# Optimization experiments

Hardware: AMD Instinct MI355X
Metric: run time of the kernel (lower is better)

The kernel has to match this reference:

```python
import jax, jax.numpy as jnp
import numpy as np
import math

B, TT, TS, C, H, L = 8, 256, 512, 512, 8, 10
HD = C // H
TOPK_FRAME = 64
# layer schedule mirrors MultimodalTransformer.forward tower order:
# 4 stimulus cross-attn (kv=frames, topk), 2 causal self-attn, 2 history cross-attn, 2 causal self-attn
# kv_source: 0=frames, 1=self, 2=id_prev
SCHED = [(0, False, TOPK_FRAME)] * 4 + [(1, True, None)] * 2 + [(2, False, None)] * 2 + [(1, True, None)] * 2


def setup_inputs() -> dict:
    key = jax.random.key(0)
    ks = jax.random.split(key, 4)
    kws = jax.random.split(ks[3], 6)
    w = lambda k, s: jax.random.normal(k, s, jnp.float32) * 0.02
    return {
        "id_x": jax.random.normal(ks[0], (B, TT, C), jnp.float32),
        "id_prev": jax.random.normal(ks[1], (B, TT, C), jnp.float32),
        "frames": jax.random.normal(ks[2], (B, TS, C), jnp.float32),
        "Wq": w(kws[0], (L, C, C)), "bq": jnp.zeros((L, C), jnp.float32),
        "Wk": w(kws[1], (L, C, C)), "bk": jnp.zeros((L, C), jnp.float32),
        "Wv": w(kws[2], (L, C, C)), "bv": jnp.zeros((L, C), jnp.float32),
        "Wo": w(kws[3], (L, C, C)), "bo": jnp.zeros((L, C), jnp.float32),
        "W1": w(kws[4], (L, C, 4 * C)), "b1": jnp.zeros((L, 4 * C), jnp.float32),
        "W2": w(kws[5], (L, 4 * C, C)), "b2": jnp.zeros((L, C), jnp.float32),
        "ln1_g": jnp.ones((L, C), jnp.float32), "ln1_b": jnp.zeros((L, C), jnp.float32),
        "ln2_g": jnp.ones((L, C), jnp.float32), "ln2_b": jnp.zeros((L, C), jnp.float32),
        "lnf_g": jnp.ones((L, C), jnp.float32), "lnf_b": jnp.zeros((L, C), jnp.float32),
    }


def _ln(x, g, b):
    mu = x.mean(-1, keepdims=True)
    var = ((x - mu) ** 2).mean(-1, keepdims=True)
    return (x - mu) * jax.lax.rsqrt(var + 1e-5) * g + b


def _block(x, kv, causal, topk, p):
    # Block.forward: x = x + attn(ln1(x), kv, kv, mask); x = x + mlp(ln2(x)); return ln_f(x)
    Wq, bq, Wk, bk, Wv, bv, Wo, bo, W1, b1, W2, b2, l1g, l1b, l2g, l2b, lfg, lfb = p
    Bx, Tt, Cx = x.shape
    Ts = kv.shape[1]
    h = _ln(x, l1g, l1b)
    q = (h @ Wq + bq).reshape(Bx, Tt, H, HD).transpose(0, 2, 1, 3)   # [B,H,Tt,HD]
    k = (kv @ Wk + bk).reshape(Bx, Ts, H, HD).transpose(0, 2, 1, 3)  # [B,H,Ts,HD]
    v = (kv @ Wv + bv).reshape(Bx, Ts, H, HD).transpose(0, 2, 1, 3)
    att = jnp.einsum('bhqd,bhkd->bhqk', q, k) * (1.0 / math.sqrt(HD))
    if causal:
        m = jnp.tril(jnp.ones((Tt, Ts), dtype=bool))
        att = jnp.where(m, att, -jnp.inf)
    if topk is not None and topk < Ts:
        top = jax.lax.top_k(att, topk)[0]           # [B,H,Tt,topk]
        att = jnp.where(att < top[..., -1:], -jnp.inf, att)
    w_att = jax.nn.softmax(att, axis=-1)
    y = jnp.einsum('bhqk,bhkd->bhqd', w_att, v).transpose(0, 2, 1, 3).reshape(Bx, Tt, Cx)
    x = x + y @ Wo + bo
    h2 = _ln(x, l2g, l2b)
    x = x + jax.nn.gelu(h2 @ W1 + b1, approximate=False) @ W2 + b2
    return _ln(x, lfg, lfb)


def _forward(id_x, id_prev, frames, Wq, bq, Wk, bk, Wv, bv, Wo, bo, W1, b1, W2, b2,
             ln1_g, ln1_b, ln2_g, ln2_b, lnf_g, lnf_b):
    x = id_x
    for i, (src, causal, topk) in enumerate(SCHED):
        kv = (frames, x, id_prev)[src]
        p = (Wq[i], bq[i], Wk[i], bk[i], Wv[i], bv[i], Wo[i], bo[i],
             W1[i], b1[i], W2[i], b2[i],
             ln1_g[i], ln1_b[i], ln2_g[i], ln2_b[i], lnf_g[i], lnf_b[i])
        x = _block(x, kv, causal, topk, p)
    return x


def reference(id_x, id_prev, frames, Wq, bq, Wk, bk, Wv, bv, Wo, bo, W1, b1, W2, b2,
              ln1_g, ln1_b, ln2_g, ln2_b, lnf_g, lnf_b):
    return _forward(id_x, id_prev, frames, Wq, bq, Wk, bk, Wv, bv, Wo, bo, W1, b1, W2, b2,
                    ln1_g, ln1_b, ln2_g, ln2_b, lnf_g, lnf_b)
```

## Files before the change

### kernel.cpp

```cpp
#include <hip/hip_runtime.h>
#include <math.h>

#define CC 512
#define NH 8
#define HD 64
#define TT 256

typedef __attribute__((ext_vector_type(8))) short short8v;
typedef __attribute__((ext_vector_type(4))) float f32x4;

__device__ inline unsigned short bfc(float f) {
  unsigned u = __float_as_uint(f);
  return (unsigned short)((u + 0x7fffu + ((u >> 16) & 1u)) >> 16);
}
__device__ inline float b2f(unsigned short s) {
  return __uint_as_float((unsigned)s << 16);
}
__device__ inline void gld16(const void* g, void* l) {
  __builtin_amdgcn_global_load_lds(
      (const __attribute__((address_space(1))) unsigned int*)g,
      (__attribute__((address_space(3))) unsigned int*)l, 16, 0, 0);
}

__global__ __launch_bounds__(256) void prep_k(const float* __restrict__ id_x,
    const float* __restrict__ frames, const float* __restrict__ id_prev,
    float* __restrict__ x, unsigned short* __restrict__ fb,
    unsigned short* __restrict__ pb) {
  int i = blockIdx.x * 256 + threadIdx.x;
  if (i < 262144) {
    ((float4*)x)[i] = ((const float4*)id_x)[i];
  } else if (i < 786432) {
    int j = i - 262144;
    float4 f = ((const float4*)frames)[j];
    ushort4 o; o.x = bfc(f.x); o.y = bfc(f.y); o.z = bfc(f.z); o.w = bfc(f.w);
    ((ushort4*)fb)[j] = o;
  } else {
    int j = i - 786432;
    float4 f = ((const float4*)id_prev)[j];
    ushort4 o; o.x = bfc(f.x); o.y = bfc(f.y); o.z = bfc(f.z); o.w = bfc(f.w);
    ((ushort4*)pb)[j] = o;
  }
}

__global__ __launch_bounds__(256) void ln_bf(const float* __restrict__ in,
    unsigned short* __restrict__ out, const float* __restrict__ g, const float* __restrict__ b) {
  int row = (blockIdx.x << 2) + (threadIdx.x >> 6), lane = threadIdx.x & 63;
  const float* r = in + (size_t)row * CC;
  float4 v0 = *(const float4*)(r + (lane << 2));
  float4 v1 = *(const float4*)(r + 256 + (lane << 2));
  float s = v0.x + v0.y + v0.z + v0.w + v1.x + v1.y + v1.z + v1.w;
  #pragma unroll
  for (int o = 32; o; o >>= 1) s += __shfl_xor(s, o);
  float mu = s * (1.0f / CC);
  float d0x = v0.x - mu, d0y = v0.y - mu, d0z = v0.z - mu, d0w = v0.w - mu;
  float d1x = v1.x - mu, d1y = v1.y - mu, d1z = v1.z - mu, d1w = v1.w - mu;
  float sq = d0x*d0x + d0y*d0y + d0z*d0z + d0w*d0w + d1x*d1x + d1y*d1y + d1z*d1z + d1w*d1w;
  #pragma unroll
  for (int o = 32; o; o >>= 1) sq += __shfl_xor(sq, o);
  float inv = rsqrtf(sq * (1.0f / CC) + 1e-5f);
  float4 g0 = *(const float4*)(g + (lane << 2)), g1 = *(const float4*)(g + 256 + (lane << 2));
  float4 b0 = *(const float4*)(b + (lane << 2)), b1 = *(const float4*)(b + 256 + (lane << 2));
  ushort4 o0, o1;
  o0.x = bfc(d0x*inv*g0.x + b0.x); o0.y = bfc(d0y*inv*g0.y + b0.y);
  o0.z = bfc(d0z*inv*g0.z + b0.z); o0.w = bfc(d0w*inv*g0.w + b0.w);
  o1.x = bfc(d1x*inv*g1.x + b1.x); o1.y = bfc(d1y*inv*g1.y + b1.y);
  o1.z = bfc(d1z*inv*g1.z + b1.z); o1.w = bfc(d1w*inv*g1.w + b1.w);
  *(ushort4*)(out + (size_t)row * CC + (lane << 2)) = o0;
  *(ushort4*)(out + (size_t)row * CC + 256 + (lane << 2)) = o1;
}

__global__ __launch_bounds__(256) void ln_final(const float* __restrict__ in,
    float* __restrict__ out, const float* __restrict__ g, const float* __restrict__ b) {
  int row = (blockIdx.x << 2) + (threadIdx.x >> 6), lane = threadIdx.x & 63;
  const float* r = in + (size_t)row * CC;
  float4 v0 = *(const float4*)(r + (lane << 2));
  float4 v1 = *(const float4*)(r + 256 + (lane << 2));
  float s = v0.x + v0.y + v0.z + v0.w + v1.x + v1.y + v1.z + v1.w;
  #pragma unroll
  for (int o = 32; o; o >>= 1) s += __shfl_xor(s, o);
  float mu = s * (1.0f / CC);
  float d0x = v0.x - mu, d0y = v0.y - mu, d0z = v0.z - mu, d0w = v0.w - mu;
  float d1x = v1.x - mu, d1y = v1.y - mu, d1z = v1.z - mu, d1w = v1.w - mu;
  float sq = d0x*d0x + d0y*d0y + d0z*d0z + d0w*d0w + d1x*d1x + d1y*d1y + d1z*d1z + d1w*d1w;
  #pragma unroll
  for (int o = 32; o; o >>= 1) sq += __shfl_xor(sq, o);
  float inv = rsqrtf(sq * (1.0f / CC) + 1e-5f);
  float4 g0 = *(const float4*)(g + (lane << 2)), g1 = *(const float4*)(g + 256 + (lane << 2));
  float4 b0 = *(const float4*)(b + (lane << 2)), b1 = *(const float4*)(b + 256 + (lane << 2));
  float4 o0, o1;
  o0.x = d0x*inv*g0.x + b0.x; o0.y = d0y*inv*g0.y + b0.y;
  o0.z = d0z*inv*g0.z + b0.z; o0.w = d0w*inv*g0.w + b0.w;
  o1.x = d1x*inv*g1.x + b1.x; o1.y = d1y*inv*g1.y + b1.y;
  o1.z = d1z*inv*g1.z + b1.z; o1.w = d1w*inv*g1.w + b1.w;
  *(float4*)(out + (size_t)row * CC + (lane << 2)) = o0;
  *(float4*)(out + (size_t)row * CC + 256 + (lane << 2)) = o1;
}

__global__ __launch_bounds__(256) void ln_chain(const float* __restrict__ in,
    float* __restrict__ xout, unsigned short* __restrict__ xb,
    const float* __restrict__ gf, const float* __restrict__ bf,
    const float* __restrict__ g1, const float* __restrict__ b1,
    unsigned short* __restrict__ hout) {
  int row = (blockIdx.x << 2) + (threadIdx.x >> 6), lane = threadIdx.x & 63;
  const float* r = in + (size_t)row * CC;
  float4 v0 = *(const float4*)(r + (lane << 2));
  float4 v1 = *(const float4*)(r + 256 + (lane << 2));
  float s = v0.x + v0.y + v0.z + v0.w + v1.x + v1.y + v1.z + v1.w;
  #pragma unroll
  for (int o = 32; o; o >>= 1) s += __shfl_xor(s, o);
  float mu = s * (1.0f / CC);
  float d0x = v0.x - mu, d0y = v0.y - mu, d0z = v0.z - mu, d0w = v0.w - mu;
  float d1x = v1.x - mu, d1y = v1.y - mu, d1z = v1.z - mu, d1w = v1.w - mu;
  float sq = d0x*d0x + d0y*d0y + d0z*d0z + d0w*d0w + d1x*d1x + d1y*d1y + d1z*d1z + d1w*d1w;
  #pragma unroll
  for (int o = 32; o; o >>= 1) sq += __shfl_xor(sq, o);
  float inv = rsqrtf(sq * (1.0f / CC) + 1e-5f);
  float4 g0 = *(const float4*)(gf + (lane << 2)), g1v = *(const float4*)(gf + 256 + (lane << 2));
  float4 b0 = *(const float4*)(bf + (lane << 2)), b1v = *(const float4*)(bf + 256 + (lane << 2));
  float4 x0, x1;
  x0.x = d0x*inv*g0.x + b0.x; x0.y = d0y*inv*g0.y + b0.y;
  x0.z = d0z*inv*g0.z + b0.z; x0.w = d0w*inv*g0.w + b0.w;
  x1.x = d1x*inv*g1v.x + b1v.x; x1.y = d1y*inv*g1v.y + b1v.y;
  x1.z = d1z*inv*g1v.z + b1v.z; x1.w = d1w*inv*g1v.w + b1v.w;
  *(float4*)(xout + (size_t)row * CC + (lane << 2)) = x0;
  *(float4*)(xout + (size_t)row * CC + 256 + (lane << 2)) = x1;
  ushort4 xb0, xb1;
  xb0.x = bfc(x0.x); xb0.y = bfc(x0.y); xb0.z = bfc(x0.z); xb0.w = bfc(x0.w);
  xb1.x = bfc(x1.x); xb1.y = bfc(x1.y); xb1.z = bfc(x1.z); xb1.w = bfc(x1.w);
  *(ushort4*)(xb + (size_t)row * CC + (lane << 2)) = xb0;
  *(ushort4*)(xb + (size_t)row * CC + 256 + (lane << 2)) = xb1;
  float s2 = x0.x + x0.y + x0.z + x0.w + x1.x + x1.y + x1.z + x1.w;
  #pragma unroll
  for (int o = 32; o; o >>= 1) s2 += __shfl_xor(s2, o);
  float mu2 = s2 * (1.0f / CC);
  float e0x = x0.x - mu2, e0y = x0.y - mu2, e0z = x0.z - mu2, e0w = x0.w - mu2;
  float e1x = x1.x - mu2, e1y = x1.y - mu2, e1z = x1.z - mu2, e1w = x1.w - mu2;
  float sq2 = e0x*e0x + e0y*e0y + e0z*e0z + e0w*e0w + e1x*e1x + e1y*e1y + e1z*e1z + e1w*e1w;
  #pragma unroll
  for (int o = 32; o; o >>= 1) sq2 += __shfl_xor(sq2, o);
  float inv2 = rsqrtf(sq2 * (1.0f / CC) + 1e-5f);
  float4 h0 = *(const float4*)(g1 + (lane << 2)), h1 = *(const float4*)(g1 + 256 + (lane << 2));
  float4 c0 = *(const float4*)(b1 + (lane << 2)), c1 = *(const float4*)(b1 + 256 + (lane << 2));
  ushort4 ho0, ho1;
  ho0.x = bfc(e0x*inv2*h0.x + c0.x); ho0.y = bfc(e0y*inv2*h0.y + c0.y);
  ho0.z = bfc(e0z*inv2*h0.z + c0.z); ho0.w = bfc(e0w*inv2*h0.w + c0.w);
  ho1.x = bfc(e1x*inv2*h1.x + c1.x); ho1.y = bfc(e1y*inv2*h1.y + c1.y);
  ho1.z = bfc(e1z*inv2*h1.z + c1.z); ho1.w = bfc(e1w*inv2*h1.w + c1.w);
  *(ushort4*)(hout + (size_t)row * CC + (lane << 2)) = ho0;
  *(ushort4*)(hout + (size_t)row * CC + 256 + (lane << 2)) = ho1;
}

__global__ __launch_bounds__(256) void transpose_w(
    const float* __restrict__ Wq, const float* __restrict__ Wk,
    const float* __restrict__ Wv, const float* __restrict__ Wo,
    const float* __restrict__ W1, const float* __restrict__ W2,
    int layer_base, unsigned short* __restrict__ wT) {
  int lz = blockIdx.x / 3072;
  int layer = layer_base + lz;
  int bid = blockIdx.x - lz * 3072;
  unsigned short* wTl = wT + (size_t)lz * 3145728;
  const float* src; unsigned short* dst; int R, Cn, tile, lg;
  if (bid < 1024) {
    int seg = bid >> 8; tile = bid & 255; R = 512; Cn = 512; lg = 4;
    const float* s4[4] = {Wq, Wk, Wv, Wo};
    src = s4[seg] + (size_t)layer * 262144;
    dst = wTl + (size_t)seg * 262144;
  } else if (bid < 2048) {
    tile = bid - 1024; R = 512; Cn = 2048; lg = 6;
    src = W1 + (size_t)layer * 1048576; dst = wTl + 1048576;
  } else {
    tile = bid - 2048; R = 2048; Cn = 512; lg = 4;
    src = W2 + (size_t)layer * 1048576; dst = wTl + 2097152;
  }
  int trb = tile >> lg, tcb = tile & ((1 << lg) - 1);
  __shared__ float tl[32][33];
  int t = threadIdx.x;
  int r = t >> 3, c4 = (t & 7) << 2;
  const float* sp = src + (size_t)(trb * 32 + r) * Cn + tcb * 32 + c4;
  float4 fv = *(const float4*)sp;
  tl[r][c4] = fv.x; tl[r][c4 + 1] = fv.y; tl[r][c4 + 2] = fv.z; tl[r][c4 + 3] = fv.w;
  __syncthreads();
  unsigned short* dp = dst + (size_t)(tcb * 32 + r) * R + trb * 32 + c4;
  ushort4 ov;
  ov.x = bfc(tl[c4][r]); ov.y = bfc(tl[c4 + 1][r]);
  ov.z = bfc(tl[c4 + 2][r]); ov.w = bfc(tl[c4 + 3][r]);
  *(ushort4*)dp = ov;
}

template<int BM, int GELU, int RES, int OUTBF, int BIAS2>
__global__ __launch_bounds__(256) void gemm_bf(
    const unsigned short* __restrict__ A, const unsigned short* __restrict__ WT,
    const float* __restrict__ bias, const float* __restrict__ bias2,
    void* __restrict__ outp, const float* __restrict__ res, int M, int N, int K) {
  __shared__ __align__(16) unsigned short As[BM * 64];
  __shared__ __align__(16) unsigned short Bs[64 * 64];
  const int tid = threadIdx.x, lane = tid & 63, wid = tid >> 6;
  const int bm = blockIdx.y * BM, bn = blockIdx.x << 6;
  const int wm = (wid >> 1) * (BM / 2), wn = (wid & 1) << 5;
  constexpr int MF = BM / 32;
  f32x4 acc[MF][2] = {};
  const int fr = lane & 15, fq = lane >> 4;
  for (int k0 = 0; k0 < K; k0 += 64) {
    if (k0) __syncthreads();
    #pragma unroll
    for (int i = 0; i < BM / 32; i++) {
      int gl = tid + (i << 8);
      int row = gl >> 3, gc = gl & 7;
      int gcs = gc ^ (row & 7);
      gld16(A + (size_t)(bm + row) * K + k0 + (gcs << 3),
            (char*)As + (i << 12) + (wid << 10));
    }
    #pragma unroll
    for (int i = 0; i < 2; i++) {
      int gl = tid + (i << 8);
      int row = gl >> 3, gc = gl & 7;
      int gcs = gc ^ (row & 7);
      gld16(WT + (size_t)(bn + row) * K + k0 + (gcs << 3),
            (char*)Bs + (i << 12) + (wid << 10));
    }
    __syncthreads();
    short8v af[MF][2], bf2[2][2];
    #pragma unroll
    for (int mf = 0; mf < MF; mf++)
      #pragma unroll
      for (int ks = 0; ks < 2; ks++) {
        int r = wm + mf * 16 + fr;
        int c = (ks << 2) + fq;
        af[mf][ks] = *(const short8v*)((const char*)As + ((((r << 7) + (c << 4))) ^ ((r & 7) << 4)));
      }
    #pragma unroll
    for (int nf = 0; nf < 2; nf++)
      #pragma unroll
      for (int ks = 0; ks < 2; ks++) {
        int r = wn + nf * 16 + fr;
        int c = (ks << 2) + fq;
        bf2[nf][ks] = *(const short8v*)((const char*)Bs + ((((r << 7) + (c << 4))) ^ ((r & 7) << 4)));
      }
    #pragma unroll
    for (int mf = 0; mf < MF; mf++)
      #pragma unroll
      for (int nf = 0; nf < 2; nf++) {
        acc[mf][nf] = __builtin_amdgcn_mfma_f32_16x16x32_bf16(af[mf][0], bf2[nf][0], acc[mf][nf], 0, 0, 0);
        acc[mf][nf] = __builtin_amdgcn_mfma_f32_16x16x32_bf16(af[mf][1], bf2[nf][1], acc[mf][nf], 0, 0, 0);
      }
  }
  #pragma unroll
  for (int mf = 0; mf < MF; mf++)
    #pragma unroll
    for (int nf = 0; nf < 2; nf++) {
      int col = bn + wn + nf * 16 + fr;
      float bia = (BIAS2 && col >= 512) ? bias2[col - 512] : bias[col];
      #pragma unroll
      for (int rr = 0; rr < 4; rr++) {
        int row = bm + wm + mf * 16 + fq * 4 + rr;
        float vv = acc[mf][nf][rr] + bia;
        if (GELU) vv = 0.5f * vv * (1.0f + erff(vv * 0.70710678118654752f));
        if (RES)  vv += res[(size_t)row * N + col];
        if (OUTBF) ((unsigned short*)outp)[(size_t)row * N + col] = bfc(vv);
        else       ((float*)outp)[(size_t)row * N + col] = vv;
      }
    }
}

template<int CAUSAL, int TOPK, int TSK>
__global__ __launch_bounds__(512, 4) void attn_m(
    const unsigned short* __restrict__ qb, const unsigned short* __restrict__ kv,
    unsigned short* __restrict__ yb) {
  constexpr int NT = TSK / 64;
  constexpr int NKC = TSK / 128;
  constexpr int SST = TSK + 8;
  __shared__ float S[8 * SST];
  __shared__ __align__(16) unsigned short Ks[128 * 64];
  __shared__ __align__(16) unsigned short Qs[16 * 64];
  __shared__ float swt[TOPK ? 8 : 1][TOPK ? 128 : 1];
  __shared__ unsigned short kidx[TOPK ? 8 : 1][TOPK ? 128 : 1];
  int tid = threadIdx.x, lane = tid & 63, wid = tid >> 6;
  int bid = blockIdx.x;
  int swz = ((bid & 7) << 8) | (bid >> 3);
  int b = swz >> 8, h = (swz >> 5) & 7, q0 = (swz & 31) << 3;
  if (tid < 128) {
    int row = tid >> 3, gc = tid & 7;
    short8v o8 = {0, 0, 0, 0, 0, 0, 0, 0};
    if (row < 8) {
      const unsigned short* qsrc = qb + (size_t)((b << 8) + q0 + row) * CC + (h << 6) + (gc << 3);
      short8v raw = *(const short8v*)qsrc;
      #pragma unroll
      for (int e = 0; e < 8; e++)
        o8[e] = (short)bfc(b2f((unsigned short)raw[e]) * 0.125f);
    }
    *(short8v*)((char*)Qs + ((tid << 4) ^ ((row & 7) << 4))) = o8;
  }
  __syncthreads();
  short8v aF[2];
  {
    int r = lane & 15, kq2 = lane >> 4;
    #pragma unroll
    for (int kc2 = 0; kc2 < 2; kc2++)
      aF[kc2] = *(const short8v*)((const char*)Qs +
                 (((r << 7) + (kc2 << 6) + (kq2 << 4)) ^ ((r & 7) << 4)));
  }
  int nte = NKC;
  if (CAUSAL) { int ub = (q0 + 8 + 127) >> 7; nte = ub < NKC ? ub : NKC; }
  const unsigned short* kgb = kv + (size_t)b * TSK * 1024 + (h << 6);
  for (int t = 0; t < nte; t++) {
    __syncthreads();
    #pragma unroll
    for (int j = 0; j < 2; j++) {
      int s = (wid << 7) + (j << 6) + lane;
      int row = s >> 3, sp = s & 7;
      gld16(kgb + (size_t)((t << 7) + row) * 1024 + ((sp ^ (row & 7)) << 3),
            (char*)Ks + (wid << 11) + (j << 10));
    }
    __syncthreads();
    int kq2 = lane >> 4;
    f32x4 acc = {};
    int key16 = (wid << 4) + (lane & 15);
    #pragma unroll
    for (int kc2 = 0; kc2 < 2; kc2++) {
      short8v bF = *(const short8v*)((const char*)Ks +
                    (((key16 << 7) + (kc2 << 6) + (kq2 << 4)) ^ ((key16 & 7) << 4)));
      acc = __builtin_amdgcn_mfma_f32_16x16x32_bf16(aF[kc2], bF, acc, 0, 0, 0);
    }
    if (kq2 < 2) {
      int col = (t << 7) + key16;
      #pragma unroll
      for (int r = 0; r < 4; r++)
        S[(kq2 * 4 + r) * SST + col] = acc[r];
    }
  }
  __syncthreads();
  int row = wid;
  int qi = q0 + row;
  int jmax = CAUSAL ? (qi + 1) : TSK;
  const unsigned short* vgb = kv + (size_t)b * TSK * 1024 + 512 + (h << 6) + lane;
  float sc[NT];
  float lmax = -3.0e38f;
  #pragma unroll
  for (int tt = 0; tt < NT; tt++) {
    int key = lane + (tt << 6);
    float v = (!CAUSAL || key < jmax) ? S[row * SST + key] : -3.0e38f;
    sc[tt] = v;
    lmax = fmaxf(lmax, v);
  }
  float mx = lmax;
  #pragma unroll
  for (int o = 32; o; o >>= 1) mx = fmaxf(mx, __shfl_xor(mx, o));
  float oacc = 0.f;
  if (TOPK) {
    unsigned key[NT];
    #pragma unroll
    for (int tt = 0; tt < NT; tt++) {
      unsigned u = __float_as_uint(sc[tt]);
      key[tt] = (u & 0x80000000u) ? ~u : (u | 0x80000000u);
    }
    unsigned prefix = 0u;
    for (int bit = 31; bit >= 0; bit--) {
      unsigned cand = prefix | (1u << bit);
      int cnt = 0;
      #pragma unroll
      for (int tt = 0; tt < NT; tt++)
        cnt += __popcll(__ballot(key[tt] >= cand));
      if (cnt >= 64) {
        prefix = cand;
        if (cnt == 64) break;
      }
    }
    float wvv[NT];
    float psum = 0.f;
    int basec = 0;
    #pragma unroll
    for (int tt = 0; tt < NT; tt++) {
      bool keep = key[tt] >= prefix;
      float wv = keep ? exp2f((sc[tt] - mx) * 1.4426950408889634f) : 0.f;
      wvv[tt] = wv;
      psum += wv;
      unsigned long long mask = __ballot(keep);
      if (keep) {
        int pos = basec + (int)__popcll(mask & ((1ull << lane) - 1ull));
        if (pos < 128) {
          kidx[row][pos] = (unsigned short)(lane + (tt << 6));
          swt[row][pos] = wv;
        }
      }
      basec += (int)__popcll(mask);
    }
    #pragma unroll
    for (int o = 32; o; o >>= 1) psum += __shfl_xor(psum, o);
    float inv = 1.0f / psum;
    int nk = basec;
    if (nk <= 128) {
      float a0 = 0.f, a1 = 0.f, a2 = 0.f, a3 = 0.f;
      int i = 0;
      for (; i + 3 < nk; i += 4) {
        a0 += swt[row][i]     * b2f(vgb[(size_t)kidx[row][i] * 1024]);
        a1 += swt[row][i + 1] * b2f(vgb[(size_t)kidx[row][i + 1] * 1024]);
        a2 += swt[row][i + 2] * b2f(vgb[(size_t)kidx[row][i + 2] * 1024]);
        a3 += swt[row][i + 3] * b2f(vgb[(size_t)kidx[row][i + 3] * 1024]);
      }
      for (; i < nk; i++) a0 += swt[row][i] * b2f(vgb[(size_t)kidx[row][i] * 1024]);
      oacc = (a0 + a1 + a2 + a3) * inv;
    } else {
      #pragma unroll
      for (int tt = 0; tt < NT; tt++)
        S[row * SST + lane + (tt << 6)] = wvv[tt];
      float a0 = 0.f, a1 = 0.f;
      for (int j = 0; j + 1 < TSK; j += 2) {
        a0 += S[row * SST + j]     * b2f(vgb[(size_t)j * 1024]);
        a1 += S[row * SST + j + 1] * b2f(vgb[(size_t)(j + 1) * 1024]);
      }
      oacc = (a0 + a1) * inv;
    }
  } else {
    float psum = 0.f;
    #pragma unroll
    for (int tt = 0; tt < NT; tt++) {
      int keyj = lane + (tt << 6);
      float wv = (keyj < jmax) ? exp2f((sc[tt] - mx) * 1.4426950408889634f) : 0.f;
      S[row * SST + keyj] = wv;
      psum += wv;
    }
    #pragma unroll
    for (int o = 32; o; o >>= 1) psum += __shfl_xor(psum, o);
    float inv = 1.0f / psum;
    float a0 = 0.f, a1 = 0.f, a2 = 0.f, a3 = 0.f;
    int j = 0;
    for (; j + 3 < jmax; j += 4) {
      a0 += S[row * SST + j]     * b2f(vgb[(size_t)j * 1024]);
      a1 += S[row * SST + j + 1] * b2f(vgb[(size_t)(j + 1) * 1024]);
      a2 += S[row * SST + j + 2] * b2f(vgb[(size_t)(j + 2) * 1024]);
      a3 += S[row * SST + j + 3] * b2f(vgb[(size_t)(j + 3) * 1024]);
    }
    for (; j < jmax; j++) a0 += S[row * SST + j] * b2f(vgb[(size_t)j * 1024]);
    oacc = (a0 + a1 + a2 + a3) * inv;
  }
  yb[(size_t)((b << 8) + qi) * CC + (h << 6) + lane] = bfc(oacc);
}

extern "C" void kernel_launch(void* const* d_in, const int* in_sizes, int n_in,
                              void* d_out, int out_size, void* d_ws, size_t ws_size,
                              hipStream_t stream) {
  const float* id_x    = (const float*)d_in[0];
  const float* id_prev = (const float*)d_in[1];
  const float* frames  = (const float*)d_in[2];
  const float* Wq = (const float*)d_in[3];  const float* bq = (const float*)d_in[4];
  const float* Wk = (const float*)d_in[5];  const float* bk = (const float*)d_in[6];
  const float* Wv = (const float*)d_in[7];  const float* bv = (const float*)d_in[8];
  const float* Wo = (const float*)d_in[9];  const float* bo = (const float*)d_in[10];
  const float* W1 = (const float*)d_in[11]; const float* b1 = (const float*)d_in[12];
  const float* W2 = (const float*)d_in[13]; const float* b2 = (const float*)d_in[14];
  const float* l1g = (const float*)d_in[15]; const float* l1b = (const float*)d_in[16];
  const float* l2g = (const float*)d_in[17]; const float* l2b = (const float*)d_in[18];
  const float* lfg = (const float*)d_in[19]; const float* lfb = (const float*)d_in[20];

  float* x = (float*)d_out;
  char* W  = (char*)d_ws;
  unsigned short* qbuf = (unsigned short*)W;
  unsigned short* kvb  = (unsigned short*)(W + ((size_t)4  << 20));
  unsigned short* m1b  = (unsigned short*)(W + ((size_t)4  << 20));
  unsigned short* hb   = (unsigned short*)(W + ((size_t)12 << 20));
  unsigned short* ybf  = (unsigned short*)(W + ((size_t)14 << 20));
  unsigned short* xb   = (unsigned short*)(W + ((size_t)16 << 20));
  unsigned short* fb   = (unsigned short*)(W + ((size_t)18 << 20));
  unsigned short* pb   = (unsigned short*)(W + ((size_t)22 << 20));
  unsigned short* wT   = (unsigned short*)(W + ((size_t)24 << 20));

  const bool allw = ws_size >= (((size_t)24 << 20) + (size_t)10 * 3145728 * 2);

  prep_k<<<4096, 256, 0, stream>>>(id_x, frames, id_prev, x, fb, pb);
  if (allw)
    transpose_w<<<30720, 256, 0, stream>>>(Wq, Wk, Wv, Wo, W1, W2, 0, wT);

  static const int ssrc[10] = {0, 0, 0, 0, 1, 1, 2, 2, 1, 1};

  for (int i = 0; i < 10; i++) {
    if (!allw)
      transpose_w<<<3072, 256, 0, stream>>>(Wq, Wk, Wv, Wo, W1, W2, i, wT);
    unsigned short* wTl = wT + (allw ? (size_t)i * 3145728 : 0);
    unsigned short* wqT = wTl;
    unsigned short* wkvT = wTl + 262144;
    unsigned short* woT = wTl + 786432;
    unsigned short* w1T = wTl + 1048576;
    unsigned short* w2T = wTl + 2097152;

    if (i == 0)
      ln_bf<<<512, 256, 0, stream>>>(x, hb, l1g, l1b);

    gemm_bf<32, 0, 0, 1, 0><<<dim3(8, 64), 256, 0, stream>>>(hb, wqT, bq + i * 512, nullptr, qbuf, nullptr, 2048, 512, 512);

    const unsigned short* kvsrc; int Mkv;
    if (ssrc[i] == 0)      { kvsrc = fb; Mkv = 4096; }
    else if (ssrc[i] == 1) { kvsrc = xb; Mkv = 2048; }
    else                   { kvsrc = pb; Mkv = 2048; }
    if (Mkv == 4096)
      gemm_bf<64, 0, 0, 1, 1><<<dim3(16, 64), 256, 0, stream>>>(kvsrc, wkvT, bk + i * 512, bv + i * 512, kvb, nullptr, 4096, 1024, 512);
    else
      gemm_bf<32, 0, 0, 1, 1><<<dim3(16, 64), 256, 0, stream>>>(kvsrc, wkvT, bk + i * 512, bv + i * 512, kvb, nullptr, 2048, 1024, 512);

    if (ssrc[i] == 0)      attn_m<0, 1, 512><<<2048, 512, 0, stream>>>(qbuf, kvb, ybf);
    else if (ssrc[i] == 1) attn_m<1, 0, 256><<<2048, 512, 0, stream>>>(qbuf, kvb, ybf);
    else                   attn_m<0, 0, 256><<<2048, 512, 0, stream>>>(qbuf, kvb, ybf);

    gemm_bf<32, 0, 1, 0, 0><<<dim3(8, 64), 256, 0, stream>>>(ybf, woT, bo + i * 512, nullptr, x, x, 2048, 512, 512);
    ln_bf<<<512, 256, 0, stream>>>(x, hb, l2g + i * 512, l2b + i * 512);
    gemm_bf<64, 1, 0, 1, 0><<<dim3(32, 32), 256, 0, stream>>>(hb, w1T, b1 + i * 2048, nullptr, m1b, nullptr, 2048, 2048, 512);
    gemm_bf<32, 0, 1, 0, 0><<<dim3(8, 64), 256, 0, stream>>>(m1b, w2T, b2 + i * 512, nullptr, x, x, 2048, 512, 2048);

    if (i < 9)
      ln_chain<<<512, 256, 0, stream>>>(x, x, xb, lfg + i * 512, lfb + i * 512,
                                        l1g + (i + 1) * 512, l1b + (i + 1) * 512, hb);
    else
      ln_final<<<512, 256, 0, stream>>>(x, x, lfg + i * 512, lfb + i * 512);
  }
}
```

Baseline: 1.006 ms.

## Double-buffer GEMM LDS staging, fold Q scaling into GEMM, enlarge transpose tiles

The GEMM kernel now uses two LDS buffers and issues the async global-to-LDS loads for the next K tile before computing the current one. This overlaps memory traffic with MFMA work and removes one barrier per iteration, at the cost of doubled shared memory, which may reduce occupancy. The 1/sqrt(HD) query scaling moves into the Q-projection GEMM epilogue, so the attention kernel loads Q straight to LDS with global_load_lds instead of converting in registers. The weight-transpose kernel switches from 32x32 to 64x64 tiles, cutting the block count fourfold.

```diff
diff --git a/kernel.cpp b/kernel.cpp
--- a/kernel.cpp
+++ b/kernel.cpp
@@ -155,70 +155,83 @@
     const float* __restrict__ Wv, const float* __restrict__ Wo,
     const float* __restrict__ W1, const float* __restrict__ W2,
     int layer_base, unsigned short* __restrict__ wT) {
-  int lz = blockIdx.x / 3072;
+  int lz = blockIdx.x / 768;
   int layer = layer_base + lz;
-  int bid = blockIdx.x - lz * 3072;
+  int bid = blockIdx.x - lz * 768;
   unsigned short* wTl = wT + (size_t)lz * 3145728;
-  const float* src; unsigned short* dst; int R, Cn, tile, lg;
-  if (bid < 1024) {
-    int seg = bid >> 8; tile = bid & 255; R = 512; Cn = 512; lg = 4;
+  const float* src; unsigned short* dst; int R, Cn, tile, lgc;
+  if (bid < 256) {
+    int seg = bid >> 6; tile = bid & 63; R = 512; Cn = 512; lgc = 3;
     const float* s4[4] = {Wq, Wk, Wv, Wo};
     src = s4[seg] + (size_t)layer * 262144;
     dst = wTl + (size_t)seg * 262144;
-  } else if (bid < 2048) {
-    tile = bid - 1024; R = 512; Cn = 2048; lg = 6;
+  } else if (bid < 512) {
+    tile = bid - 256; R = 512; Cn = 2048; lgc = 5;
     src = W1 + (size_t)layer * 1048576; dst = wTl + 1048576;
   } else {
-    tile = bid - 2048; R = 2048; Cn = 512; lg = 4;
+    tile = bid - 512; R = 2048; Cn = 512; lgc = 3;
     src = W2 + (size_t)layer * 1048576; dst = wTl + 2097152;
   }
-  int trb = tile >> lg, tcb = tile & ((1 << lg) - 1);
-  __shared__ float tl[32][33];
+  int trb = tile >> lgc, tcb = tile & ((1 << lgc) - 1);
+  __shared__ float tl[64][65];
   int t = threadIdx.x;
-  int r = t >> 3, c4 = (t & 7) << 2;
-  const float* sp = src + (size_t)(trb * 32 + r) * Cn + tcb * 32 + c4;
-  float4 fv = *(const float4*)sp;
-  tl[r][c4] = fv.x; tl[r][c4 + 1] = fv.y; tl[r][c4 + 2] = fv.z; tl[r][c4 + 3] = fv.w;
+  int r = t >> 2, c0 = (t & 3) << 4;
+  const float* sp = src + (size_t)(trb * 64 + r) * Cn + tcb * 64 + c0;
+  #pragma unroll
+  for (int j = 0; j < 4; j++) {
+    float4 fv = *(const float4*)(sp + (j << 2));
+    tl[r][c0 + (j << 2)]     = fv.x; tl[r][c0 + (j << 2) + 1] = fv.y;
+    tl[r][c0 + (j << 2) + 2] = fv.z; tl[r][c0 + (j << 2) + 3] = fv.w;
+  }
   __syncthreads();
-  unsigned short* dp = dst + (size_t)(tcb * 32 + r) * R + trb * 32 + c4;
-  ushort4 ov;
-  ov.x = bfc(tl[c4][r]); ov.y = bfc(tl[c4 + 1][r]);
-  ov.z = bfc(tl[c4 + 2][r]); ov.w = bfc(tl[c4 + 3][r]);
-  *(ushort4*)dp = ov;
-}
-
-template<int BM, int GELU, int RES, int OUTBF, int BIAS2>
+  unsigned short* dp = dst + (size_t)(tcb * 64 + r) * R + trb * 64 + c0;
+  #pragma unroll
+  for (int j = 0; j < 4; j++) {
+    ushort4 ov;
+    ov.x = bfc(tl[c0 + (j << 2)][r]);     ov.y = bfc(tl[c0 + (j << 2) + 1][r]);
+    ov.z = bfc(tl[c0 + (j << 2) + 2][r]); ov.w = bfc(tl[c0 + (j << 2) + 3][r]);
+    *(ushort4*)(dp + (j << 2)) = ov;
+  }
+}
+
+template<int BM, int GELU, int RES, int OUTBF, int BIAS2, int QSC>
 __global__ __launch_bounds__(256) void gemm_bf(
     const unsigned short* __restrict__ A, const unsigned short* __restrict__ WT,
     const float* __restrict__ bias, const float* __restrict__ bias2,
     void* __restrict__ outp, const float* __restrict__ res, int M, int N, int K) {
-  __shared__ __align__(16) unsigned short As[BM * 64];
-  __shared__ __align__(16) unsigned short Bs[64 * 64];
+  __shared__ __align__(16) unsigned short As[2][BM * 64];
+  __shared__ __align__(16) unsigned short Bs[2][64 * 64];
   const int tid = threadIdx.x, lane = tid & 63, wid = tid >> 6;
   const int bm = blockIdx.y * BM, bn = blockIdx.x << 6;
   const int wm = (wid >> 1) * (BM / 2), wn = (wid & 1) << 5;
   constexpr int MF = BM / 32;
   f32x4 acc[MF][2] = {};
   const int fr = lane & 15, fq = lane >> 4;
+  const int srow_a = tid >> 3, sgc = tid & 7;
+  const int sgcs = sgc ^ (srow_a & 7);
+
+  auto stage = [&](int buf, int k0) {
+    #pragma unroll
+    for (int i = 0; i < BM / 32; i++) {
+      int row = srow_a + (i << 5);
+      int gcs = sgc ^ (row & 7);
+      gld16(A + (size_t)(bm + row) * K + k0 + (gcs << 3),
+            (char*)As[buf] + (i << 12) + (wid << 10));
+    }
+    #pragma unroll
+    for (int i = 0; i < 2; i++) {
+      int row = srow_a + (i << 5);
+      int gcs = sgc ^ (row & 7);
+      gld16(WT + (size_t)(bn + row) * K + k0 + (gcs << 3),
+            (char*)Bs[buf] + (i << 12) + (wid << 10));
+    }
+  };
+
+  stage(0, 0);
+  __syncthreads();
+  int cur = 0;
   for (int k0 = 0; k0 < K; k0 += 64) {
-    if (k0) __syncthreads();
-    #pragma unroll
-    for (int i = 0; i < BM / 32; i++) {
-      int gl = tid + (i << 8);
-      int row = gl >> 3, gc = gl & 7;
-      int gcs = gc ^ (row & 7);
-      gld16(A + (size_t)(bm + row) * K + k0 + (gcs << 3),
-            (char*)As + (i << 12) + (wid << 10));
-    }
-    #pragma unroll
-    for (int i = 0; i < 2; i++) {
-      int gl = tid + (i << 8);
-      int row = gl >> 3, gc = gl & 7;
-      int gcs = gc ^ (row & 7);
-      gld16(WT + (size_t)(bn + row) * K + k0 + (gcs << 3),
-            (char*)Bs + (i << 12) + (wid << 10));
-    }
-    __syncthreads();
+    if (k0 + 64 < K) stage(cur ^ 1, k0 + 64);
     short8v af[MF][2], bf2[2][2];
     #pragma unroll
     for (int mf = 0; mf < MF; mf++)
@@ -226,7 +239,7 @@
       for (int ks = 0; ks < 2; ks++) {
         int r = wm + mf * 16 + fr;
         int c = (ks << 2) + fq;
-        af[mf][ks] = *(const short8v*)((const char*)As + ((((r << 7) + (c << 4))) ^ ((r & 7) << 4)));
+        af[mf][ks] = *(const short8v*)((const char*)As[cur] + ((((r << 7) + (c << 4))) ^ ((r & 7) << 4)));
       }
     #pragma unroll
     for (int nf = 0; nf < 2; nf++)
@@ -234,7 +247,7 @@
       for (int ks = 0; ks < 2; ks++) {
         int r = wn + nf * 16 + fr;
         int c = (ks << 2) + fq;
-        bf2[nf][ks] = *(const short8v*)((const char*)Bs + ((((r << 7) + (c << 4))) ^ ((r & 7) << 4)));
+        bf2[nf][ks] = *(const short8v*)((const char*)Bs[cur] + ((((r << 7) + (c << 4))) ^ ((r & 7) << 4)));
       }
     #pragma unroll
     for (int mf = 0; mf < MF; mf++)
@@ -243,6 +256,8 @@
         acc[mf][nf] = __builtin_amdgcn_mfma_f32_16x16x32_bf16(af[mf][0], bf2[nf][0], acc[mf][nf], 0, 0, 0);
         acc[mf][nf] = __builtin_amdgcn_mfma_f32_16x16x32_bf16(af[mf][1], bf2[nf][1], acc[mf][nf], 0, 0, 0);
       }
+    __syncthreads();
+    cur ^= 1;
   }
   #pragma unroll
   for (int mf = 0; mf < MF; mf++)
@@ -256,6 +271,7 @@
         float vv = acc[mf][nf][rr] + bia;
         if (GELU) vv = 0.5f * vv * (1.0f + erff(vv * 0.70710678118654752f));
         if (RES)  vv += res[(size_t)row * N + col];
+        if (QSC)  vv *= 0.125f;
         if (OUTBF) ((unsigned short*)outp)[(size_t)row * N + col] = bfc(vv);
         else       ((float*)outp)[(size_t)row * N + col] = vv;
       }
@@ -278,17 +294,13 @@
   int bid = blockIdx.x;
   int swz = ((bid & 7) << 8) | (bid >> 3);
   int b = swz >> 8, h = (swz >> 5) & 7, q0 = (swz & 31) << 3;
-  if (tid < 128) {
-    int row = tid >> 3, gc = tid & 7;
-    short8v o8 = {0, 0, 0, 0, 0, 0, 0, 0};
-    if (row < 8) {
-      const unsigned short* qsrc = qb + (size_t)((b << 8) + q0 + row) * CC + (h << 6) + (gc << 3);
-      short8v raw = *(const short8v*)qsrc;
-      #pragma unroll
-      for (int e = 0; e < 8; e++)
-        o8[e] = (short)bfc(b2f((unsigned short)raw[e]) * 0.125f);
-    }
-    *(short8v*)((char*)Qs + ((tid << 4) ^ ((row & 7) << 4))) = o8;
+  if (tid < 64) {
+    int row = tid >> 3, sp = tid & 7;
+    gld16(qb + (size_t)((b << 8) + q0 + row) * CC + (h << 6) + ((sp ^ (row & 7)) << 3),
+          (char*)Qs);
+  } else if (tid < 128) {
+    short8v z = {0, 0, 0, 0, 0, 0, 0, 0};
+    *(short8v*)((char*)Qs + (tid << 4)) = z;
   }
   __syncthreads();
   short8v aF[2];
@@ -468,13 +480,13 @@
 
   prep_k<<<4096, 256, 0, stream>>>(id_x, frames, id_prev, x, fb, pb);
   if (allw)
-    transpose_w<<<30720, 256, 0, stream>>>(Wq, Wk, Wv, Wo, W1, W2, 0, wT);
+    transpose_w<<<7680, 256, 0, stream>>>(Wq, Wk, Wv, Wo, W1, W2, 0, wT);
 
   static const int ssrc[10] = {0, 0, 0, 0, 1, 1, 2, 2, 1, 1};
 
   for (int i = 0; i < 10; i++) {
     if (!allw)
-      transpose_w<<<3072, 256, 0, stream>>>(Wq, Wk, Wv, Wo, W1, W2, i, wT);
+      transpose_w<<<768, 256, 0, stream>>>(Wq, Wk, Wv, Wo, W1, W2, i, wT);
     unsigned short* wTl = wT + (allw ? (size_t)i * 3145728 : 0);
     unsigned short* wqT = wTl;
     unsigned short* wkvT = wTl + 262144;
@@ -485,25 +497,25 @@
     if (i == 0)
       ln_bf<<<512, 256, 0, stream>>>(x, hb, l1g, l1b);
 
-    gemm_bf<32, 0, 0, 1, 0><<<dim3(8, 64), 256, 0, stream>>>(hb, wqT, bq + i * 512, nullptr, qbuf, nullptr, 2048, 512, 512);
+    gemm_bf<32, 0, 0, 1, 0, 1><<<dim3(8, 64), 256, 0, stream>>>(hb, wqT, bq + i * 512, nullptr, qbuf, nullptr, 2048, 512, 512);
 
     const unsigned short* kvsrc; int Mkv;
     if (ssrc[i] == 0)      { kvsrc = fb; Mkv = 4096; }
     else if (ssrc[i] == 1) { kvsrc = xb; Mkv = 2048; }
     else                   { kvsrc = pb; Mkv = 2048; }
     if (Mkv == 4096)
-      gemm_bf<64, 0, 0, 1, 1><<<dim3(16, 64), 256, 0, stream>>>(kvsrc, wkvT, bk + i * 512, bv + i * 512, kvb, nullptr, 4096, 1024, 512);
+      gemm_bf<64, 0, 0, 1, 1, 0><<<dim3(16, 64), 256, 0, stream>>>(kvsrc, wkvT, bk + i * 512, bv + i * 512, kvb, nullptr, 4096, 1024, 512);
     else
-      gemm_bf<32, 0, 0, 1, 1><<<dim3(16, 64), 256, 0, stream>>>(kvsrc, wkvT, bk + i * 512, bv + i * 512, kvb, nullptr, 2048, 1024, 512);
+      gemm_bf<32, 0, 0, 1, 1, 0><<<dim3(16, 64), 256, 0, stream>>>(kvsrc, wkvT, bk + i * 512, bv + i * 512, kvb, nullptr, 2048, 1024, 512);
 
     if (ssrc[i] == 0)      attn_m<0, 1, 512><<<2048, 512, 0, stream>>>(qbuf, kvb, ybf);
     else if (ssrc[i] == 1) attn_m<1, 0, 256><<<2048, 512, 0, stream>>>(qbuf, kvb, ybf);
     else                   attn_m<0, 0, 256><<<2048, 512, 0, stream>>>(qbuf, kvb, ybf);
 
-    gemm_bf<32, 0, 1, 0, 0><<<dim3(8, 64), 256, 0, stream>>>(ybf, woT, bo + i * 512, nullptr, x, x, 2048, 512, 512);
+    gemm_bf<32, 0, 1, 0, 0, 0><<<dim3(8, 64), 256, 0, stream>>>(ybf, woT, bo + i * 512, nullptr, x, x, 2048, 512, 512);
     ln_bf<<<512, 256, 0, stream>>>(x, hb, l2g + i * 512, l2b + i * 512);
-    gemm_bf<64, 1, 0, 1, 0><<<dim3(32, 32), 256, 0, stream>>>(hb, w1T, b1 + i * 2048, nullptr, m1b, nullptr, 2048, 2048, 512);
-    gemm_bf<32, 0, 1, 0, 0><<<dim3(8, 64), 256, 0, stream>>>(m1b, w2T, b2 + i * 512, nullptr, x, x, 2048, 512, 2048);
+    gemm_bf<64, 1, 0, 1, 0, 0><<<dim3(32, 32), 256, 0, stream>>>(hb, w1T, b1 + i * 2048, nullptr, m1b, nullptr, 2048, 2048, 512);
+    gemm_bf<32, 0, 1, 0, 0, 0><<<dim3(8, 64), 256, 0, stream>>>(m1b, w2T, b2 + i * 512, nullptr, x, x, 2048, 512, 2048);
 
     if (i < 9)
       ln_chain<<<512, 256, 0, stream>>>(x, x, xb, lfg + i * 512, lfb + i * 512,
```

Measured after the change: 1.037 ms. +3.1%, slower.
